# Optimization experiments

Measured on AMD Instinct MI355X. Metric: run time of the kernel, lower is better.

## Reference

```python
import jax, jax.numpy as jnp
import numpy as np

M, K, N = 8192, 4096, 4096  # tokens, in_features, out_features


def setup_inputs() -> dict:
    key = jax.random.key(0)
    k1, k2, k3, k4, k5, k6 = jax.random.split(key, 6)
    return {
        "x_q": jax.random.randint(k1, (M, K), 0, 256, dtype=jnp.int32),
        "weight_int8": jax.random.randint(k2, (N, K), 0, 256, dtype=jnp.int32),
        "weight_scale": jax.random.uniform(k3, (N, 1), dtype=jnp.float32) * 0.01 + 1e-4,
        "weight_zero_point": jax.random.randint(k4, (N, 1), 0, 256, dtype=jnp.int32),
        "bias": jax.random.normal(k5, (N,), dtype=jnp.float32),
        "input_scale": jax.random.uniform(k6, (1,), dtype=jnp.float32) * 0.05 + 1e-4,
        "input_zero_point": 128,
    }


def reference(x_q, weight_int8, weight_scale, weight_zero_point, bias, input_scale, input_zero_point):
    # zero-point-subtracted fp32 operands (simulated int32 accumulation in fp32)
    x_f = x_q.astype(jnp.float32) - jnp.float32(input_zero_point)      # [M, K]
    w_f = weight_int8.astype(jnp.float32) - weight_zero_point.astype(jnp.float32)  # [N, K]
    acc = jnp.einsum('mk,nk->mn', x_f, w_f)                            # [M, N]
    dequant_scale = input_scale * weight_scale.T                       # [1, N]
    return acc * dequant_scale + bias                                  # [M, N]
```

## Files before the change

kernel.cpp:

```cpp
#include <hip/hip_runtime.h>
#include <hip/hip_bf16.h>
#include <stdint.h>

typedef int v4i  __attribute__((ext_vector_type(4)));
typedef int v16i __attribute__((ext_vector_type(16)));

#define AS_GLOBAL(p) ((const __attribute__((address_space(1))) void*)(p))
#define AS_LDS(p)    ((__attribute__((address_space(3))) void*)(p))

__global__ __launch_bounds__(256) void prep_x_kernel(const int* __restrict__ x,
                                                     const int* __restrict__ izp_p,
                                                     signed char* __restrict__ xs,
                                                     int* __restrict__ rowsum, int K) {
    int row = blockIdx.x;
    int izp = izp_p[0];
    const int4* xr = (const int4*)(x + (long)row * K);
    uint32_t* xo = (uint32_t*)(xs + (long)row * K);
    int sum = 0;
    int n4 = K >> 2;
    for (int i = threadIdx.x; i < n4; i += 256) {
        int4 v = xr[i];
        int a0 = v.x - izp, a1 = v.y - izp, a2 = v.z - izp, a3 = v.w - izp;
        sum += a0 + a1 + a2 + a3;
        xo[i] = (uint32_t)(a0 & 0xFF) | ((uint32_t)(a1 & 0xFF) << 8) |
                ((uint32_t)(a2 & 0xFF) << 16) | ((uint32_t)(a3 & 0xFF) << 24);
    }
    sum += __shfl_down(sum, 32);
    sum += __shfl_down(sum, 16);
    sum += __shfl_down(sum, 8);
    sum += __shfl_down(sum, 4);
    sum += __shfl_down(sum, 2);
    sum += __shfl_down(sum, 1);
    __shared__ int red[4];
    if ((threadIdx.x & 63) == 0) red[threadIdx.x >> 6] = sum;
    __syncthreads();
    if (threadIdx.x == 0) rowsum[row] = red[0] + red[1] + red[2] + red[3];
}

__global__ __launch_bounds__(256) void prep_w_kernel(const int* __restrict__ w,
                                                     signed char* __restrict__ ws, int K) {
    int row = blockIdx.x;
    const int4* wr = (const int4*)(w + (long)row * K);
    uint32_t* wo = (uint32_t*)(ws + (long)row * K);
    int n4 = K >> 2;
    for (int i = threadIdx.x; i < n4; i += 256) {
        int4 v = wr[i];
        int a0 = v.x - 128, a1 = v.y - 128, a2 = v.z - 128, a3 = v.w - 128;
        wo[i] = (uint32_t)(a0 & 0xFF) | ((uint32_t)(a1 & 0xFF) << 8) |
                ((uint32_t)(a2 & 0xFF) << 16) | ((uint32_t)(a3 & 0xFF) << 24);
    }
}


#define BAR  __builtin_amdgcn_s_barrier()
#define PHASE_END do { asm volatile("s_waitcnt lgkmcnt(0)" ::: "memory"); \
                       __builtin_amdgcn_sched_barrier(0); BAR; } while (0)
#define VM4  asm volatile("s_waitcnt vmcnt(4)" ::: "memory")
#define PRIO1 __builtin_amdgcn_s_setprio(1)
#define PRIO0 __builtin_amdgcn_s_setprio(0)

#define STAGE(gbase, opofs, half, buf, tile) do {                                     \
    int t_ = (tile); if (t_ >= NT) t_ -= NT;                                          \
    const signed char* src_ = (gbase) + (long)((half) * 128) * K + (long)t_ * 128;    \
    signed char* dst_ = ldsw + (buf) * 65536 + (opofs) + (half) * 16384;              \
    __builtin_amdgcn_global_load_lds(AS_GLOBAL(src_), AS_LDS(dst_), 16, 0, 0);        \
    __builtin_amdgcn_global_load_lds(AS_GLOBAL(src_ + 64L * K), AS_LDS(dst_ + 8192), 16, 0, 0); \
  } while (0)

#define READ_A(buf, mi, ks)                                                           \
    af[mi][ks] = *(const v4i*)(lds + (buf) * 65536 + abase##mi + (kc##ks << 4));
#define READ_B(buf, ni, ks)                                                           \
    bf[ni][ks] = *(const v4i*)(lds + (buf) * 65536 + bbase##ni + (kc##ks << 4));

#define MM(mi, ni, ks)                                                                 \
    acc[(mi)*2+(ni)] = __builtin_amdgcn_mfma_i32_32x32x32_i8(af[mi][ks], bf[ni][ks],  \
                                                             acc[(mi)*2+(ni)], 0, 0, 0);
#define MFMA8(m0, m1, k0, k1) do {                                                     \
    MM(m0, 0, k0) MM(m0, 1, k0) MM(m1, 0, k0) MM(m1, 1, k0)                            \
    MM(m0, 0, k1) MM(m0, 1, k1) MM(m1, 0, k1) MM(m1, 1, k1) } while (0)

#define KTILE(b, tA, tB) do {                                                          \
                                                                              \
    READ_A(b, 0, 0) READ_A(b, 1, 0) READ_B(b, 0, 0) READ_B(b, 1, 0)                    \
    READ_A(b, 0, 1) READ_A(b, 1, 1) READ_B(b, 0, 1) READ_B(b, 1, 1)                    \
    STAGE(gA, 0, 0, (b) ^ 1, tA);                                                      \
    BAR;                                                                               \
    PRIO1; MFMA8(0, 1, 0, 1); PRIO0;                                                   \
    PHASE_END;                                                                         \
                                                                              \
    READ_A(b, 0, 2) READ_A(b, 1, 2) READ_B(b, 0, 2) READ_B(b, 1, 2)                    \
    READ_A(b, 0, 3) READ_A(b, 1, 3) READ_B(b, 0, 3) READ_B(b, 1, 3)                    \
    STAGE(gA, 0, 1, (b) ^ 1, tA);                                                      \
    BAR;                                                                               \
    PRIO1; MFMA8(0, 1, 2, 3); PRIO0;                                                   \
    PHASE_END;                                                                         \
                                                                              \
    READ_A(b, 2, 0) READ_A(b, 3, 0) READ_A(b, 2, 1) READ_A(b, 3, 1)                    \
    STAGE(gB, 32768, 0, (b), tB);                                                      \
    BAR;                                                                               \
    PRIO1; MFMA8(2, 3, 0, 1); PRIO0;                                                   \
    PHASE_END;                                                                         \
                                                                              \
    READ_A(b, 2, 2) READ_A(b, 3, 2) READ_A(b, 2, 3) READ_A(b, 3, 3)                    \
    STAGE(gB, 32768, 1, (b), tB);                                                      \
    BAR;                                                                               \
    PRIO1; MFMA8(2, 3, 2, 3); PRIO0; VM4;                                              \
    PHASE_END;                                                                         \
  } while (0)

__global__ __launch_bounds__(512, 2) void gemm_i8_8ph(
    const signed char* __restrict__ A,
    const signed char* __restrict__ B,
    const int* __restrict__ rowsum, const float* __restrict__ wscale,
    const int* __restrict__ wzp, const float* __restrict__ bias,
    const float* __restrict__ iscale, float* __restrict__ C,
    int M, int N, int K) {
  __shared__ signed char lds[131072];
  const int tid = threadIdx.x;
  const int w = tid >> 6, l = tid & 63;
  const int wm = w >> 2, wn = w & 3;

  int nwg = gridDim.x, bid = blockIdx.x;
  if ((nwg & 7) == 0) { int cpx = nwg >> 3; bid = (bid & 7) * cpx + (bid >> 3); }
  const int ntiles = N >> 8;
  const int mt = bid / ntiles, nt = bid - mt * ntiles;
  const long brow = (long)mt << 8, bcol = (long)nt << 8;

  const int NT = K >> 7;
  const int NI = NT >> 1;

  const int srow = w * 8 + (l >> 3);
  const int schunk = ((l & 7) ^ (l >> 3)) << 4;
  const signed char* gA = A + (brow + srow) * (long)K + schunk;
  const signed char* gB = B + (bcol + srow) * (long)K + schunk;
  signed char* ldsw = lds + w * 1024;

  const int lr = l & 31, hi = l >> 5, xr = l & 7;
  const int abase0 = (wm * 128 + 0  * 32 + lr) * 128;
  const int abase1 = (wm * 128 + 1  * 32 + lr) * 128;
  const int abase2 = (wm * 128 + 2  * 32 + lr) * 128;
  const int abase3 = (wm * 128 + 3  * 32 + lr) * 128;
  const int bbase0 = 32768 + (wn * 64 + 0 * 32 + lr) * 128;
  const int bbase1 = 32768 + (wn * 64 + 1 * 32 + lr) * 128;
  const int kc0 = (0 * 2 + hi) ^ xr;
  const int kc1 = (1 * 2 + hi) ^ xr;
  const int kc2 = (2 * 2 + hi) ^ xr;
  const int kc3 = (3 * 2 + hi) ^ xr;

  v16i acc[8] = {};
  v4i af[4][4], bf[2][4];

  STAGE(gB, 32768, 0, 0, 0); STAGE(gB, 32768, 1, 0, 0);
  STAGE(gA, 0, 0, 0, 0);     STAGE(gA, 0, 1, 0, 0);
  STAGE(gB, 32768, 0, 1, 1); STAGE(gB, 32768, 1, 1, 1);
  VM4; BAR;

  for (int i = 0; i < NI; ++i) {
    const int t1 = 2 * i + 1, t2 = 2 * i + 2, t3 = 2 * i + 3;
    KTILE(0, t1, t2);
    KTILE(1, t2, t3);
  }

  const float is = iscale[0];
  int rs[4][16];
#pragma unroll
  for (int mi = 0; mi < 4; ++mi)
#pragma unroll
    for (int reg = 0; reg < 16; ++reg)
      rs[mi][reg] = rowsum[(int)brow + wm * 128 + mi * 32 + (reg & 3) + 8 * (reg >> 2) + 4 * hi];
#pragma unroll
  for (int ni = 0; ni < 2; ++ni) {
    const int col = (int)bcol + wn * 64 + ni * 32 + lr;
    const float sc = is * wscale[col];
    const int zpc = 128 - wzp[col];
    const float bi = bias[col];
#pragma unroll
    for (int mi = 0; mi < 4; ++mi) {
#pragma unroll
      for (int reg = 0; reg < 16; ++reg) {
        const int row = (int)brow + wm * 128 + mi * 32 + (reg & 3) + 8 * (reg >> 2) + 4 * hi;
        const int v = acc[mi * 2 + ni][reg] + zpc * rs[mi][reg];
        C[(long)row * N + col] = (float)v * sc + bi;
      }
    }
  }
}

extern "C" void kernel_launch(void* const* d_in, const int* in_sizes, int n_in,
                              void* d_out, int out_size, void* d_ws, size_t ws_size,
                              hipStream_t stream) {
    const int* x_q = (const int*)d_in[0];
    const int* w_q = (const int*)d_in[1];
    const float* wscale = (const float*)d_in[2];
    const int* wzp = (const int*)d_in[3];
    const float* bias = (const float*)d_in[4];
    const float* iscale = (const float*)d_in[5];
    const int* izp = (const int*)d_in[6];

    int N = in_sizes[2];
    int K = in_sizes[1] / N;
    int M = in_sizes[0] / K;

    signed char* xs = (signed char*)d_ws;
    signed char* wsq = xs + (size_t)M * K;
    int* rowsum = (int*)(wsq + (size_t)N * K);

    prep_x_kernel<<<M, 256, 0, stream>>>(x_q, izp, xs, rowsum, K);
    prep_w_kernel<<<N, 256, 0, stream>>>(w_q, wsq, K);

    int grid = (M / 256) * (N / 256);
    gemm_i8_8ph<<<grid, 512, 0, stream>>>(xs, wsq, rowsum, wscale, wzp, bias, iscale,
                                          (float*)d_out, M, N, K);
}
```

Measured before the change: 217.0 us.

## Software-pipeline LDS fragment reads with MFMA using partial lgkmcnt waits

Restructures the int8 GEMM K-tile loop so LDS fragment loads for the next phase are issued before the current phase's MFMAs, using two alternating A-fragment register sets and partial lgkmcnt waits instead of a full wait plus sched_barrier each phase. Barriers drop from two per phase to one. The goal is to hide LDS read latency behind matrix-core work and cut synchronization stalls. The partial waits assume a particular order in which the LDS reads complete, so a wrong count could silently read stale fragments. It may also change register pressure under the 2-waves occupancy bound.

```diff
diff --git a/kernel.cpp b/kernel.cpp
--- a/kernel.cpp
+++ b/kernel.cpp
@@ -53,8 +53,7 @@
 
 
 #define BAR  __builtin_amdgcn_s_barrier()
-#define PHASE_END do { asm volatile("s_waitcnt lgkmcnt(0)" ::: "memory"); \
-                       __builtin_amdgcn_sched_barrier(0); BAR; } while (0)
+#define LGKM(n) asm volatile("s_waitcnt lgkmcnt(" #n ")" ::: "memory")
 #define VM4  asm volatile("s_waitcnt vmcnt(4)" ::: "memory")
 #define PRIO1 __builtin_amdgcn_s_setprio(1)
 #define PRIO0 __builtin_amdgcn_s_setprio(0)
@@ -67,45 +66,53 @@
     __builtin_amdgcn_global_load_lds(AS_GLOBAL(src_ + 64L * K), AS_LDS(dst_ + 8192), 16, 0, 0); \
   } while (0)
 
-#define READ_A(buf, mi, ks)                                                           \
-    af[mi][ks] = *(const v4i*)(lds + (buf) * 65536 + abase##mi + (kc##ks << 4));
-#define READ_B(buf, ni, ks)                                                           \
-    bf[ni][ks] = *(const v4i*)(lds + (buf) * 65536 + bbase##ni + (kc##ks << 4));
-
-#define MM(mi, ni, ks)                                                                 \
-    acc[(mi)*2+(ni)] = __builtin_amdgcn_mfma_i32_32x32x32_i8(af[mi][ks], bf[ni][ks],  \
-                                                             acc[(mi)*2+(ni)], 0, 0, 0);
-#define MFMA8(m0, m1, k0, k1) do {                                                     \
-    MM(m0, 0, k0) MM(m0, 1, k0) MM(m1, 0, k0) MM(m1, 1, k0)                            \
-    MM(m0, 0, k1) MM(m0, 1, k1) MM(m1, 0, k1) MM(m1, 1, k1) } while (0)
+#define LDF(b, base, kc) (*(const v4i*)(lds + (b) * 65536 + (base) + ((kc) << 4)))
+
+#define RD_BF01(b) do {                                                                \
+    bf[0][0] = LDF(b, bbase0, kc0); bf[1][0] = LDF(b, bbase1, kc0);                    \
+    bf[0][1] = LDF(b, bbase0, kc1); bf[1][1] = LDF(b, bbase1, kc1); } while (0)
+#define RD_BF23(b) do {                                                                \
+    bf[0][2] = LDF(b, bbase0, kc2); bf[1][2] = LDF(b, bbase1, kc2);                    \
+    bf[0][3] = LDF(b, bbase0, kc3); bf[1][3] = LDF(b, bbase1, kc3); } while (0)
+#define RD_SET(dst, b, ba0, ba1, c0, c1) do {                                          \
+    dst[0][0] = LDF(b, ba0, c0); dst[1][0] = LDF(b, ba1, c0);                          \
+    dst[0][1] = LDF(b, ba0, c1); dst[1][1] = LDF(b, ba1, c1); } while (0)
+
+#define MP(SET, i, ni, j, kb, mb)                                                      \
+    acc[((mb) + (i)) * 2 + (ni)] = __builtin_amdgcn_mfma_i32_32x32x32_i8(              \
+        SET[i][j], bf[ni][(kb) + (j)], acc[((mb) + (i)) * 2 + (ni)], 0, 0, 0);
+#define MFMA_PH(SET, kb, mb) do {                                                      \
+    MP(SET, 0, 0, 0, kb, mb) MP(SET, 0, 1, 0, kb, mb)                                  \
+    MP(SET, 1, 0, 0, kb, mb) MP(SET, 1, 1, 0, kb, mb)                                  \
+    MP(SET, 0, 0, 1, kb, mb) MP(SET, 0, 1, 1, kb, mb)                                  \
+    MP(SET, 1, 0, 1, kb, mb) MP(SET, 1, 1, 1, kb, mb) } while (0)
 
 #define KTILE(b, tA, tB) do {                                                          \
-                                                                              \
-    READ_A(b, 0, 0) READ_A(b, 1, 0) READ_B(b, 0, 0) READ_B(b, 1, 0)                    \
-    READ_A(b, 0, 1) READ_A(b, 1, 1) READ_B(b, 0, 1) READ_B(b, 1, 1)                    \
+                                   \
+    RD_BF01(b); RD_SET(afA, b, abase0, abase1, kc0, kc1);                              \
+    RD_SET(afB, b, abase0, abase1, kc2, kc3);                                          \
     STAGE(gA, 0, 0, (b) ^ 1, tA);                                                      \
-    BAR;                                                                               \
-    PRIO1; MFMA8(0, 1, 0, 1); PRIO0;                                                   \
-    PHASE_END;                                                                         \
-                                                                              \
-    READ_A(b, 0, 2) READ_A(b, 1, 2) READ_B(b, 0, 2) READ_B(b, 1, 2)                    \
-    READ_A(b, 0, 3) READ_A(b, 1, 3) READ_B(b, 0, 3) READ_B(b, 1, 3)                    \
+    LGKM(4);                                        \
+    PRIO1; MFMA_PH(afA, 0, 0); PRIO0;                                                  \
+    BAR;                                                                               \
+                                               \
+    RD_BF23(b); RD_SET(afA, b, abase2, abase3, kc0, kc1);                              \
     STAGE(gA, 0, 1, (b) ^ 1, tA);                                                      \
-    BAR;                                                                               \
-    PRIO1; MFMA8(0, 1, 2, 3); PRIO0;                                                   \
-    PHASE_END;                                                                         \
-                                                                              \
-    READ_A(b, 2, 0) READ_A(b, 3, 0) READ_A(b, 2, 1) READ_A(b, 3, 1)                    \
+    LGKM(4);                                       \
+    PRIO1; MFMA_PH(afB, 2, 0); PRIO0;                                                  \
+    BAR;                                                                               \
+           \
+    RD_SET(afB, b, abase2, abase3, kc2, kc3);                                          \
+    LGKM(4);                                           \
     STAGE(gB, 32768, 0, (b), tB);                                                      \
-    BAR;                                                                               \
-    PRIO1; MFMA8(2, 3, 0, 1); PRIO0;                                                   \
-    PHASE_END;                                                                         \
-                                                                              \
-    READ_A(b, 2, 2) READ_A(b, 3, 2) READ_A(b, 2, 3) READ_A(b, 3, 3)                    \
+    PRIO1; MFMA_PH(afA, 0, 2); PRIO0;                                                  \
+    BAR;                                                                               \
+                                                                    \
     STAGE(gB, 32768, 1, (b), tB);                                                      \
-    BAR;                                                                               \
-    PRIO1; MFMA8(2, 3, 2, 3); PRIO0; VM4;                                              \
-    PHASE_END;                                                                         \
+    LGKM(0);                    \
+    PRIO1; MFMA_PH(afB, 2, 2); PRIO0;                                                  \
+    VM4;                                                                               \
+    BAR;                                                                               \
   } while (0)
 
 __global__ __launch_bounds__(512, 2) void gemm_i8_8ph(
@@ -136,10 +143,10 @@
   signed char* ldsw = lds + w * 1024;
 
   const int lr = l & 31, hi = l >> 5, xr = l & 7;
-  const int abase0 = (wm * 128 + 0  * 32 + lr) * 128;
-  const int abase1 = (wm * 128 + 1  * 32 + lr) * 128;
-  const int abase2 = (wm * 128 + 2  * 32 + lr) * 128;
-  const int abase3 = (wm * 128 + 3  * 32 + lr) * 128;
+  const int abase0 = (wm * 128 + 0 * 32 + lr) * 128;
+  const int abase1 = (wm * 128 + 1 * 32 + lr) * 128;
+  const int abase2 = (wm * 128 + 2 * 32 + lr) * 128;
+  const int abase3 = (wm * 128 + 3 * 32 + lr) * 128;
   const int bbase0 = 32768 + (wn * 64 + 0 * 32 + lr) * 128;
   const int bbase1 = 32768 + (wn * 64 + 1 * 32 + lr) * 128;
   const int kc0 = (0 * 2 + hi) ^ xr;
@@ -148,7 +155,8 @@
   const int kc3 = (3 * 2 + hi) ^ xr;
 
   v16i acc[8] = {};
-  v4i af[4][4], bf[2][4];
+  v4i afA[2][2], afB[2][2];
+  v4i bf[2][4];
 
   STAGE(gB, 32768, 0, 0, 0); STAGE(gB, 32768, 1, 0, 0);
   STAGE(gA, 0, 0, 0, 0);     STAGE(gA, 0, 1, 0, 0);
```

Result: slower. 252.1 us (+16.2%).
